# Optimization experiments

Measured on AMD Instinct MI355X. Metric: run time of the kernel, lower is better.

The kernel has to match this reference:

```python
import jax, jax.numpy as jnp
import numpy as np

B, S, D = 32, 512, 768
M, T = 32, 30
H, DFF, L, E = 12, 3072, 4, 100000
HD = D // H


def _layer_norm(x, w, b):
    m = jnp.mean(x, axis=-1, keepdims=True)
    v = jnp.var(x, axis=-1, keepdims=True)
    return (x - m) * jax.lax.rsqrt(v + 1e-5) * w + b


def _encoder_layer(x, p):
    # torch.nn.TransformerEncoderLayer, batch_first, post-LN, relu, eval (no dropout)
    wi, bi, wo, bo, g1, b1, w1, c1, w2, c2, g2, b2 = p
    qkv = x @ wi.T + bi                                   # [B,M,3D]
    q, k, v = jnp.split(qkv, 3, axis=-1)
    q = q.reshape(B, M, H, HD)
    k = k.reshape(B, M, H, HD)
    v = v.reshape(B, M, H, HD)
    a = jnp.einsum('bqhd,bkhd->bhqk', q, k) / np.float32(np.sqrt(HD))
    a = jax.nn.softmax(a, axis=-1)
    o = jnp.einsum('bhqk,bkhd->bqhd', a, v).reshape(B, M, D)
    x = _layer_norm(x + o @ wo.T + bo, g1, b1)
    ff = jax.nn.relu(x @ w1.T + c1) @ w2.T + c2
    return _layer_norm(x + ff, g2, b2)


def _forward(lhs, attn_w, attn_b, Wi, Bi, Wo, Bo, G1, B1, W1, C1, W2, C2, G2, B2v,
             cls_w1, cls_w2, cls_b2, pos, emask):
    # Vectorized form of the source triple loop: token slot x of mention (i,j) is
    # copied from last_hidden_state[i, x] while no -1 has been seen (break) and
    # the mention is active (entity_attention_mask != 0).
    valid = jnp.cumprod((pos != -1).astype(jnp.int32), axis=-1) > 0      # [B,M,T]
    valid = valid & (emask[:, :, None] != 0)
    mentions = jnp.where(valid[..., None], lhs[:, None, :T, :], 0.0)     # [B,M,T,D]
    scores = jax.nn.softmax(jnp.einsum('bmtd,d->bmt', mentions, attn_w) + attn_b, axis=-1)
    x = jnp.einsum('bmt,bmtd->bmd', scores, mentions)                    # attention pool
    for l in range(L):
        x = _encoder_layer(x, (Wi[l], Bi[l], Wo[l], Bo[l], G1[l], B1[l],
                               W1[l], C1[l], W2[l], C2[l], G2[l], B2v[l]))
    return (x @ cls_w1.T) @ cls_w2.T + cls_b2                            # [B,M,E]


def setup_inputs() -> dict:
    key = jax.random.key(0)
    k = jax.random.split(key, 12)
    lhs = jax.random.normal(k[0], (B, S, D), jnp.float32)
    pos = jax.random.randint(k[1], (B, M, T), 0, S)
    lens = jax.random.randint(k[2], (B, M), 0, T + 1)
    pos = jnp.where(jnp.arange(T)[None, None, :] < lens[..., None], pos, -1)
    emask = jax.random.randint(k[3], (B, M), 0, 2)
    s = 0.02
    return {
        'last_hidden_state': lhs,
        'attn_w': jax.random.normal(k[4], (D,), jnp.float32) * s,
        'attn_b': jnp.zeros((), jnp.float32),
        'in_proj_w': jax.random.normal(k[5], (L, 3 * D, D), jnp.float32) * s,
        'in_proj_b': jnp.zeros((L, 3 * D), jnp.float32),
        'out_w': jax.random.normal(k[6], (L, D, D), jnp.float32) * s,
        'out_b': jnp.zeros((L, D), jnp.float32),
        'ln1_w': jnp.ones((L, D), jnp.float32),
        'ln1_b': jnp.zeros((L, D), jnp.float32),
        'lin1_w': jax.random.normal(k[7], (L, DFF, D), jnp.float32) * s,
        'lin1_b': jnp.zeros((L, DFF), jnp.float32),
        'lin2_w': jax.random.normal(k[8], (L, D, DFF), jnp.float32) * s,
        'lin2_b': jnp.zeros((L, D), jnp.float32),
        'ln2_w': jnp.ones((L, D), jnp.float32),
        'ln2_b': jnp.zeros((L, D), jnp.float32),
        'cls_w1': jax.random.normal(k[9], (100, D), jnp.float32) * s,
        'cls_w2': jax.random.normal(k[10], (E, 100), jnp.float32) * s,
        'cls_b2': jnp.zeros((E,), jnp.float32),
        'entity_position_ids': pos,
        'entity_attention_mask': emask,
    }


def reference(last_hidden_state, attn_w, attn_b, in_proj_w, in_proj_b, out_w, out_b,
              ln1_w, ln1_b, lin1_w, lin1_b, lin2_w, lin2_b, ln2_w, ln2_b,
              cls_w1, cls_w2, cls_b2, entity_position_ids, entity_attention_mask):
    return _forward(last_hidden_state, attn_w, attn_b, in_proj_w, in_proj_b, out_w, out_b,
                    ln1_w, ln1_b, lin1_w, lin1_b, lin2_w, lin2_b, ln2_w, ln2_b,
                    cls_w1, cls_w2, cls_b2, entity_position_ids, entity_attention_mask)
```

## Files before the change

kernel.cpp:

```cpp
#include <hip/hip_runtime.h>

constexpr int Bc = 32, Sc = 512, Dc = 768, Mc = 32, Tc = 30;
constexpr int Hc = 12, DFFc = 3072, Lc = 4, Ec = 100000, HDc = 64;
constexpr int TOK = Bc * Mc;
constexpr int KC2 = 128;

typedef float floatx4 __attribute__((ext_vector_type(4)));
typedef __bf16 bfrag8 __attribute__((ext_vector_type(8)));
typedef unsigned short usx8 __attribute__((ext_vector_type(8)));
typedef unsigned short usx4 __attribute__((ext_vector_type(4)));

__device__ __forceinline__ unsigned short f32_to_bf16(float f) {
    unsigned int u = __float_as_uint(f);
    unsigned int r = (u + 0x7FFFu + ((u >> 16) & 1u)) >> 16;
    return (unsigned short)r;
}

__device__ __forceinline__ void gload_lds16(const void* gsrc, void* lds) {
    __builtin_amdgcn_global_load_lds((const unsigned int*)gsrc, (unsigned int*)lds, 16, 0, 0);
}

struct CvtSegs {
    const float* src[7];
    unsigned short* dst[7];
    unsigned int end[7];
    unsigned int total;
};

__global__ __launch_bounds__(256)
void cvt_multi_kernel(CvtSegs a) {
    const unsigned int stride = gridDim.x * 256;
    for (unsigned int i = blockIdx.x * 256 + threadIdx.x; i < a.total; i += stride) {
        int s = 0;
        while (i >= a.end[s]) ++s;
        const unsigned int off = i - (s ? a.end[s - 1] : 0u);
        usx4 o = (usx4)0;
        if (a.src[s]) {
            floatx4 v = *(const floatx4*)(a.src[s] + 4 * (size_t)off);
            #pragma unroll
            for (int j = 0; j < 4; ++j) o[j] = f32_to_bf16(v[j]);
        }
        *(usx4*)(a.dst[s] + 4 * (size_t)off) = o;
    }
}

__global__ __launch_bounds__(256)
void cvt_c2_kernel(const float* __restrict__ src, unsigned short* __restrict__ dst) {
    const int total = Ec * (KC2 / 8);
    const int stride = gridDim.x * 256;
    for (int c = blockIdx.x * 256 + threadIdx.x; c < total; c += stride) {
        const int row = c >> 4, j = c & 15;
        const int col0 = j * 8;
        const float* sp = src + (size_t)row * 100 + col0;
        usx8 o = (usx8)0;
        if (col0 + 8 <= 100) {
            floatx4 v0 = *(const floatx4*)(sp);
            floatx4 v1 = *(const floatx4*)(sp + 4);
            #pragma unroll
            for (int jj = 0; jj < 4; ++jj) { o[jj] = f32_to_bf16(v0[jj]); o[4 + jj] = f32_to_bf16(v1[jj]); }
        } else if (col0 < 100) {
            #pragma unroll
            for (int jj = 0; jj < 8; ++jj)
                if (col0 + jj < 100) o[jj] = f32_to_bf16(sp[jj]);
        }
        *(usx8*)(dst + (size_t)row * KC2 + col0) = o;
    }
}

__global__ __launch_bounds__(256)
void pool_kernel(const float* __restrict__ lhs, const float* __restrict__ attn_w,
                 const int* __restrict__ pos, const int* __restrict__ emask,
                 float* __restrict__ x0, unsigned short* __restrict__ x0b) {
    const int bm = blockIdx.x;
    const int b = bm >> 5;
    const int tid = threadIdx.x;
    __shared__ float s_logit[32];
    __shared__ float s_w[32];
    __shared__ int s_valid[32];

    if (tid == 0) {
        int em = emask[bm];
        int ok = 1;
        for (int t = 0; t < Tc; ++t) {
            if (pos[bm * Tc + t] == -1) ok = 0;
            s_valid[t] = (ok && em) ? 1 : 0;
        }
    }
    __syncthreads();

    const int wid = tid >> 6, lane = tid & 63;
    for (int t = wid; t < Tc; t += 4) {
        float p = 0.f;
        const float* row = lhs + ((size_t)b * Sc + t) * Dc;
        for (int d = lane; d < Dc; d += 64) p += row[d] * attn_w[d];
        #pragma unroll
        for (int off = 32; off > 0; off >>= 1) p += __shfl_down(p, off);
        if (lane == 0) s_logit[t] = s_valid[t] ? p : 0.0f;
    }
    __syncthreads();
    if (tid == 0) {
        float mx = -1e30f;
        for (int t = 0; t < Tc; ++t) mx = fmaxf(mx, s_logit[t]);
        float sum = 0.f;
        for (int t = 0; t < Tc; ++t) { float e = expf(s_logit[t] - mx); s_w[t] = e; sum += e; }
        float inv = 1.0f / sum;
        for (int t = 0; t < Tc; ++t) s_w[t] = s_valid[t] ? s_w[t] * inv : 0.0f;
    }
    __syncthreads();
    for (int d = tid; d < Dc; d += 256) {
        float acc = 0.f;
        for (int t = 0; t < Tc; ++t) acc += s_w[t] * lhs[((size_t)b * Sc + t) * Dc + d];
        x0[(size_t)bm * Dc + d] = acc;
        x0b[(size_t)bm * Dc + d] = f32_to_bf16(acc);
    }
}

template <int BM, int BN, int WM, int WN, int OUTBF>
__global__ __launch_bounds__(256)
void gemm_bf16_kernel(const unsigned short* __restrict__ A, int lda,
                      const unsigned short* __restrict__ B, int ldb,
                      const float* __restrict__ bias, void* __restrict__ Cv,
                      int ldc, int M, int N, int K, int relu, int nxReal) {
    constexpr int BK = 64;
    __shared__ unsigned short lA[BM * BK];
    __shared__ unsigned short lB[BN * BK];

    int bx, by;
    if (nxReal > 0) {
        const int gx = gridDim.x, gy = gridDim.y;
        const int lb = blockIdx.y * gx + blockIdx.x;
        const int xcd = lb & 7, p = lb >> 3;
        const int pq = p / gy;
        bx = xcd * (gx >> 3) + pq;
        by = p - pq * gy;
        if (bx >= nxReal) return;
    } else {
        bx = blockIdx.x; by = blockIdx.y;
    }
    const int z = blockIdx.z;
    A += (size_t)z * K;
    B += (size_t)z * K;

    const int tid = threadIdx.x;
    const int bm0 = by * BM;
    const int bn0 = bx * BN;

    const int wid = tid >> 6;
    const int lane = tid & 63;
    const int quad = lane >> 4;
    const int l16 = lane & 15;
    const int wr = (wid >> 1) * (WM * 16);
    const int wc = (wid & 1) * (WN * 16);

    floatx4 acc[WM][WN] = {};

    for (int k0 = 0; k0 < K; k0 += BK) {
        #pragma unroll
        for (int it = 0; it < BM / 32; ++it) {
            const int chunk = wid * (BM / 32) + it;
            const int boff = chunk * 1024 + lane * 16;
            const int row = boff >> 7;
            const int cb = (boff & 127) ^ ((row & 7) << 4);
            gload_lds16((const char*)(A + (size_t)(bm0 + row) * lda + k0) + cb,
                        &lA[chunk * 512]);
        }
        #pragma unroll
        for (int it = 0; it < BN / 32; ++it) {
            const int chunk = wid * (BN / 32) + it;
            const int boff = chunk * 1024 + lane * 16;
            const int row = boff >> 7;
            const int cb = (boff & 127) ^ ((row & 7) << 4);
            gload_lds16((const char*)(B + (size_t)(bn0 + row) * ldb + k0) + cb,
                        &lB[chunk * 512]);
        }
        __syncthreads();
        #pragma unroll
        for (int kk = 0; kk < BK; kk += 32) {
            bfrag8 af[WM], bfr[WN];
            #pragma unroll
            for (int i = 0; i < WM; ++i) {
                const int rowA = wr + i * 16 + l16;
                af[i] = *(const bfrag8*)((const char*)lA + rowA * 128 +
                                         ((kk * 2 + quad * 16) ^ ((rowA & 7) << 4)));
            }
            #pragma unroll
            for (int j = 0; j < WN; ++j) {
                const int rowB = wc + j * 16 + l16;
                bfr[j] = *(const bfrag8*)((const char*)lB + rowB * 128 +
                                          ((kk * 2 + quad * 16) ^ ((rowB & 7) << 4)));
            }
            #pragma unroll
            for (int i = 0; i < WM; ++i)
                #pragma unroll
                for (int j = 0; j < WN; ++j)
                    acc[i][j] = __builtin_amdgcn_mfma_f32_16x16x32_bf16(af[i], bfr[j], acc[i][j], 0, 0, 0);
        }
        __syncthreads();
    }

    #pragma unroll
    for (int i = 0; i < WM; ++i) {
        #pragma unroll
        for (int j = 0; j < WN; ++j) {
            const int col = bn0 + wc + j * 16 + l16;
            if (col < N) {
                const int row0 = bm0 + wr + i * 16 + quad * 4;
                const float bv = bias ? bias[col] : 0.0f;
                #pragma unroll
                for (int r = 0; r < 4; ++r) {
                    float v = acc[i][j][r] + bv;
                    if (relu) v = fmaxf(v, 0.0f);
                    const size_t idx = (size_t)z * M * ldc + (size_t)(row0 + r) * ldc + col;
                    if (OUTBF) ((unsigned short*)Cv)[idx] = f32_to_bf16(v);
                    else       ((float*)Cv)[idx] = v;
                }
            }
        }
    }
}

__global__ __launch_bounds__(256)
void attn_kernel(const float* __restrict__ qkv, unsigned short* __restrict__ outb) {
    const int bh = blockIdx.x;
    const int b = bh / Hc, h = bh % Hc;
    const int tid = threadIdx.x;
    __shared__ float sQ[32][65];
    __shared__ float sK[32][65];
    __shared__ float sV[32][65];
    __shared__ float sS[32][33];

    const int m = tid >> 3;
    const int c0 = (tid & 7) * 8;
    {
        const size_t rbase = ((size_t)(b * 32 + m)) * (3 * Dc);
        #pragma unroll
        for (int j = 0; j < 8; ++j) {
            sQ[m][c0 + j] = qkv[rbase + h * HDc + c0 + j];
            sK[m][c0 + j] = qkv[rbase + Dc + h * HDc + c0 + j];
            sV[m][c0 + j] = qkv[rbase + 2 * Dc + h * HDc + c0 + j];
        }
    }
    __syncthreads();

    #pragma unroll
    for (int u = 0; u < 4; ++u) {
        const int e = tid * 4 + u;
        const int q = e >> 5, k = e & 31;
        float s = 0.f;
        #pragma unroll
        for (int d = 0; d < HDc; ++d) s += sQ[q][d] * sK[k][d];
        sS[q][k] = s * 0.125f;
    }
    __syncthreads();
    if (tid < 32) {
        float mx = -1e30f;
        for (int k = 0; k < 32; ++k) mx = fmaxf(mx, sS[tid][k]);
        float sum = 0.f;
        for (int k = 0; k < 32; ++k) { float e = expf(sS[tid][k] - mx); sS[tid][k] = e; sum += e; }
        const float inv = 1.0f / sum;
        for (int k = 0; k < 32; ++k) sS[tid][k] *= inv;
    }
    __syncthreads();
    float o[8] = {};
    for (int k = 0; k < 32; ++k) {
        const float p = sS[m][k];
        #pragma unroll
        for (int j = 0; j < 8; ++j) o[j] += p * sV[k][c0 + j];
    }
    usx8 o8;
    #pragma unroll
    for (int j = 0; j < 8; ++j) o8[j] = f32_to_bf16(o[j]);
    *(usx8*)(&outb[((size_t)(b * 32 + m)) * Dc + h * HDc + c0]) = o8;
}

__global__ __launch_bounds__(256)
void addln_kernel(const float* __restrict__ xa, const float* __restrict__ xs, int nslab,
                  const float* __restrict__ badd, const float* __restrict__ g,
                  const float* __restrict__ be, float* __restrict__ outf,
                  unsigned short* __restrict__ outb) {
    const int row = blockIdx.x;
    const int tid = threadIdx.x;
    __shared__ float red[8];
    float v[3];
    float s = 0.f, sq = 0.f;
    #pragma unroll
    for (int i = 0; i < 3; ++i) {
        const int d = tid + i * 256;
        float x = xa[(size_t)row * Dc + d] + badd[d];
        for (int sl = 0; sl < nslab; ++sl)
            x += xs[((size_t)sl * TOK + row) * Dc + d];
        v[i] = x; s += x; sq += x * x;
    }
    #pragma unroll
    for (int off = 32; off > 0; off >>= 1) {
        s += __shfl_down(s, off);
        sq += __shfl_down(sq, off);
    }
    if ((tid & 63) == 0) { red[tid >> 6] = s; red[4 + (tid >> 6)] = sq; }
    __syncthreads();
    const float ts = red[0] + red[1] + red[2] + red[3];
    const float tq = red[4] + red[5] + red[6] + red[7];
    const float mean = ts * (1.0f / Dc);
    const float var = tq * (1.0f / Dc) - mean * mean;
    const float inv = rsqrtf(var + 1e-5f);
    #pragma unroll
    for (int i = 0; i < 3; ++i) {
        const int d = tid + i * 256;
        const float y = (v[i] - mean) * inv * g[d] + be[d];
        outf[(size_t)row * Dc + d] = y;
        outb[(size_t)row * Dc + d] = f32_to_bf16(y);
    }
}

extern "C" void kernel_launch(void* const* d_in, const int* in_sizes, int n_in,
                              void* d_out, int out_size, void* d_ws, size_t ws_size,
                              hipStream_t stream) {
    const float* lhs   = (const float*)d_in[0];
    const float* attnw = (const float*)d_in[1];
    const float* ipw = (const float*)d_in[3];
    const float* ipb = (const float*)d_in[4];
    const float* oww = (const float*)d_in[5];
    const float* owb = (const float*)d_in[6];
    const float* g1  = (const float*)d_in[7];
    const float* b1  = (const float*)d_in[8];
    const float* l1w = (const float*)d_in[9];
    const float* l1b = (const float*)d_in[10];
    const float* l2w = (const float*)d_in[11];
    const float* l2b = (const float*)d_in[12];
    const float* g2  = (const float*)d_in[13];
    const float* b2  = (const float*)d_in[14];
    const float* cw1 = (const float*)d_in[15];
    const float* cw2 = (const float*)d_in[16];
    const float* cb2 = (const float*)d_in[17];
    const int* pos   = (const int*)d_in[18];
    const int* emask = (const int*)d_in[19];
    float* out = (float*)d_out;

    constexpr size_t N_IP = (size_t)Lc * 3 * Dc * Dc;
    constexpr size_t N_OW = (size_t)Lc * Dc * Dc;
    constexpr size_t N_L1 = (size_t)Lc * DFFc * Dc;
    constexpr size_t N_L2 = (size_t)Lc * Dc * DFFc;
    constexpr size_t N_C1 = (size_t)KC2 * Dc;

    char* ws = (char*)d_ws;
    unsigned short* bw_c2 = (unsigned short*)ws;
    unsigned short* bufCb = bw_c2 + (size_t)Ec * KC2;

    constexpr size_t F_XA   = (size_t)TOK * Dc;
    constexpr size_t F_QKV  = (size_t)TOK * 3 * Dc;
    constexpr size_t F_SLAB = (size_t)4 * TOK * Dc;
    constexpr size_t S_ACT  = (size_t)TOK * Dc;
    constexpr size_t S_FFH  = (size_t)TOK * DFFc;
    constexpr size_t tail_bytes =
        4 * (F_XA + F_XA + F_QKV + F_SLAB) +
        2 * (N_IP + N_OW + N_L1 + N_L2 + N_C1 + 3 * S_ACT + S_FFH);

    const size_t out_bytes = (size_t)out_size * 4;
    char* tail = (char*)d_out + ((out_bytes - tail_bytes) & ~(size_t)255);

    float* xA   = (float*)tail;
    float* xB   = xA + F_XA;
    float* qkvb = xB + F_XA;
    float* bufS = qkvb + F_QKV;
    unsigned short* bw_ip = (unsigned short*)(bufS + F_SLAB);
    unsigned short* bw_ow = bw_ip + N_IP;
    unsigned short* bw_l1 = bw_ow + N_OW;
    unsigned short* bw_l2 = bw_l1 + N_L1;
    unsigned short* bw_c1 = bw_l2 + N_L2;
    unsigned short* xAb   = bw_c1 + N_C1;
    unsigned short* xBb   = xAb + S_ACT;
    unsigned short* attnb = xBb + S_ACT;
    unsigned short* bufHb = attnb + S_ACT;

    {
        CvtSegs segs{};
        const float* srcs[6] = {ipw, oww, l1w, l2w, cw1, nullptr};
        unsigned short* dsts[6] = {bw_ip, bw_ow, bw_l1, bw_l2, bw_c1, bw_c1 + (size_t)100 * Dc};
        const unsigned int cnt[6] = {(unsigned)(N_IP / 4), (unsigned)(N_OW / 4),
                                     (unsigned)(N_L1 / 4), (unsigned)(N_L2 / 4),
                                     (unsigned)(100 * Dc / 4), (unsigned)(28 * Dc / 4)};
        unsigned int acc = 0;
        for (int i = 0; i < 6; ++i) { segs.src[i] = srcs[i]; segs.dst[i] = dsts[i]; acc += cnt[i]; segs.end[i] = acc; }
        segs.src[6] = nullptr; segs.dst[6] = dsts[5]; segs.end[6] = 0xFFFFFFFFu;
        segs.total = acc;
        cvt_multi_kernel<<<2048, 256, 0, stream>>>(segs);
    }
    cvt_c2_kernel<<<1024, 256, 0, stream>>>(cw2, bw_c2);

    pool_kernel<<<TOK, 256, 0, stream>>>(lhs, attnw, pos, emask, xA, xAb);

    auto g64 = [&](const unsigned short* A, int lda, const unsigned short* B, int ldb,
                   const float* bias, void* C, int ldc, int N, int K, int relu,
                   int ks, int outbf, bool swz) {
        int gx = (N + 63) / 64, nx = -1;
        if (swz) { nx = gx; gx = (gx + 7) & ~7; }
        dim3 grid(gx, TOK / 64, ks);
        if (outbf) gemm_bf16_kernel<64, 64, 2, 2, 1><<<grid, 256, 0, stream>>>(A, lda, B, ldb, bias, C, ldc, TOK, N, K, relu, nx);
        else       gemm_bf16_kernel<64, 64, 2, 2, 0><<<grid, 256, 0, stream>>>(A, lda, B, ldb, bias, C, ldc, TOK, N, K, relu, nx);
    };

    for (int l = 0; l < Lc; ++l) {
        g64(xAb, Dc, bw_ip + (size_t)l * 3 * Dc * Dc, Dc, ipb + (size_t)l * 3 * Dc,
            qkvb, 3 * Dc, 3 * Dc, Dc, 0, 1, 0, false);
        attn_kernel<<<Bc * Hc, 256, 0, stream>>>(qkvb, attnb);
        g64(attnb, Dc, bw_ow + (size_t)l * Dc * Dc, Dc, nullptr,
            bufS, Dc, Dc, Dc / 4, 0, 4, 0, false);
        addln_kernel<<<TOK, 256, 0, stream>>>(xA, bufS, 4, owb + (size_t)l * Dc,
                                              g1 + (size_t)l * Dc, b1 + (size_t)l * Dc, xB, xBb);
        g64(xBb, Dc, bw_l1 + (size_t)l * DFFc * Dc, Dc, l1b + (size_t)l * DFFc,
            bufHb, DFFc, DFFc, Dc, 1, 1, 1, true);
        g64(bufHb, DFFc, bw_l2 + (size_t)l * Dc * DFFc, DFFc, nullptr,
            bufS, Dc, Dc, DFFc / 4, 0, 4, 0, false);
        addln_kernel<<<TOK, 256, 0, stream>>>(xB, bufS, 4, l2b + (size_t)l * Dc,
                                              g2 + (size_t)l * Dc, b2 + (size_t)l * Dc, xA, xAb);
    }

    g64(xAb, Dc, bw_c1, Dc, nullptr, bufCb, KC2, KC2, Dc, 0, 1, 1, false);
    {
        int nx = (Ec + 127) / 128;
        int gx = (nx + 7) & ~7;
        dim3 grid(gx, TOK / 128, 1);
        gemm_bf16_kernel<128, 128, 4, 4, 0><<<grid, 256, 0, stream>>>(
            bufCb, KC2, bw_c2, KC2, cb2, out, Ec, TOK, Ec, KC2, 0, nx);
    }
}
```

Baseline: 1.000 ms.

## Merge front conversion/pool kernels and double-buffer GEMM LDS tiles

Combines the two weight-conversion kernels and the mention pooling kernel into one launch, with blocks split by index range, which removes two launches and lets the independent work run side by side. The GEMM kernel also gets double-buffered LDS: the next K tile is loaded with global_load_lds while MFMA runs on the current tile, and one barrier per iteration is dropped. This doubles LDS use per block, which may lower occupancy. There is no explicit wait on the asynchronous LDS loads before the barrier, so correctness relies on the compiler inserting the right waitcnt.

```diff
diff --git a/kernel.cpp b/kernel.cpp
--- a/kernel.cpp
+++ b/kernel.cpp
@@ -27,53 +27,57 @@
     unsigned int total;
 };
 
+constexpr int FB_CVT1 = 1536, FB_CVT2 = 512, FB_POOL = TOK;
+
 __global__ __launch_bounds__(256)
-void cvt_multi_kernel(CvtSegs a) {
-    const unsigned int stride = gridDim.x * 256;
-    for (unsigned int i = blockIdx.x * 256 + threadIdx.x; i < a.total; i += stride) {
-        int s = 0;
-        while (i >= a.end[s]) ++s;
-        const unsigned int off = i - (s ? a.end[s - 1] : 0u);
-        usx4 o = (usx4)0;
-        if (a.src[s]) {
-            floatx4 v = *(const floatx4*)(a.src[s] + 4 * (size_t)off);
-            #pragma unroll
-            for (int j = 0; j < 4; ++j) o[j] = f32_to_bf16(v[j]);
-        }
-        *(usx4*)(a.dst[s] + 4 * (size_t)off) = o;
-    }
-}
-
-__global__ __launch_bounds__(256)
-void cvt_c2_kernel(const float* __restrict__ src, unsigned short* __restrict__ dst) {
-    const int total = Ec * (KC2 / 8);
-    const int stride = gridDim.x * 256;
-    for (int c = blockIdx.x * 256 + threadIdx.x; c < total; c += stride) {
-        const int row = c >> 4, j = c & 15;
-        const int col0 = j * 8;
-        const float* sp = src + (size_t)row * 100 + col0;
-        usx8 o = (usx8)0;
-        if (col0 + 8 <= 100) {
-            floatx4 v0 = *(const floatx4*)(sp);
-            floatx4 v1 = *(const floatx4*)(sp + 4);
-            #pragma unroll
-            for (int jj = 0; jj < 4; ++jj) { o[jj] = f32_to_bf16(v0[jj]); o[4 + jj] = f32_to_bf16(v1[jj]); }
-        } else if (col0 < 100) {
-            #pragma unroll
-            for (int jj = 0; jj < 8; ++jj)
-                if (col0 + jj < 100) o[jj] = f32_to_bf16(sp[jj]);
-        }
-        *(usx8*)(dst + (size_t)row * KC2 + col0) = o;
-    }
-}
-
-__global__ __launch_bounds__(256)
-void pool_kernel(const float* __restrict__ lhs, const float* __restrict__ attn_w,
-                 const int* __restrict__ pos, const int* __restrict__ emask,
-                 float* __restrict__ x0, unsigned short* __restrict__ x0b) {
-    const int bm = blockIdx.x;
+void front_kernel(CvtSegs a, const float* __restrict__ cw2, unsigned short* __restrict__ bw_c2,
+                  const float* __restrict__ lhs, const float* __restrict__ attn_w,
+                  const int* __restrict__ pos, const int* __restrict__ emask,
+                  float* __restrict__ x0, unsigned short* __restrict__ x0b) {
+    const int bid = blockIdx.x;
+    const int tid = threadIdx.x;
+
+    if (bid < FB_CVT1) {
+        const unsigned int stride = FB_CVT1 * 256;
+        for (unsigned int i = bid * 256 + tid; i < a.total; i += stride) {
+            int s = 0;
+            while (i >= a.end[s]) ++s;
+            const unsigned int off = i - (s ? a.end[s - 1] : 0u);
+            usx4 o = (usx4)0;
+            if (a.src[s]) {
+                floatx4 v = *(const floatx4*)(a.src[s] + 4 * (size_t)off);
+                #pragma unroll
+                for (int j = 0; j < 4; ++j) o[j] = f32_to_bf16(v[j]);
+            }
+            *(usx4*)(a.dst[s] + 4 * (size_t)off) = o;
+        }
+        return;
+    }
+    if (bid < FB_CVT1 + FB_CVT2) {
+        const int total = Ec * (KC2 / 8);
+        const int stride = FB_CVT2 * 256;
+        for (int c = (bid - FB_CVT1) * 256 + tid; c < total; c += stride) {
+            const int row = c >> 4, j = c & 15;
+            const int col0 = j * 8;
+            const float* sp = cw2 + (size_t)row * 100 + col0;
+            usx8 o = (usx8)0;
+            if (col0 + 8 <= 100) {
+                floatx4 v0 = *(const floatx4*)(sp);
+                floatx4 v1 = *(const floatx4*)(sp + 4);
+                #pragma unroll
+                for (int jj = 0; jj < 4; ++jj) { o[jj] = f32_to_bf16(v0[jj]); o[4 + jj] = f32_to_bf16(v1[jj]); }
+            } else if (col0 < 100) {
+                #pragma unroll
+                for (int jj = 0; jj < 8; ++jj)
+                    if (col0 + jj < 100) o[jj] = f32_to_bf16(sp[jj]);
+            }
+            *(usx8*)(bw_c2 + (size_t)row * KC2 + col0) = o;
+        }
+        return;
+    }
+
+    const int bm = bid - (FB_CVT1 + FB_CVT2);
     const int b = bm >> 5;
-    const int tid = threadIdx.x;
     __shared__ float s_logit[32];
     __shared__ float s_w[32];
     __shared__ int s_valid[32];
@@ -122,8 +126,8 @@
                       const float* __restrict__ bias, void* __restrict__ Cv,
                       int ldc, int M, int N, int K, int relu, int nxReal) {
     constexpr int BK = 64;
-    __shared__ unsigned short lA[BM * BK];
-    __shared__ unsigned short lB[BN * BK];
+    __shared__ unsigned short lA[2][BM * BK];
+    __shared__ unsigned short lB[2][BN * BK];
 
     int bx, by;
     if (nxReal > 0) {
@@ -154,7 +158,7 @@
 
     floatx4 acc[WM][WN] = {};
 
-    for (int k0 = 0; k0 < K; k0 += BK) {
+    auto stageA = [&](int buf, int k0) {
         #pragma unroll
         for (int it = 0; it < BM / 32; ++it) {
             const int chunk = wid * (BM / 32) + it;
@@ -162,8 +166,10 @@
             const int row = boff >> 7;
             const int cb = (boff & 127) ^ ((row & 7) << 4);
             gload_lds16((const char*)(A + (size_t)(bm0 + row) * lda + k0) + cb,
-                        &lA[chunk * 512]);
-        }
+                        &lA[buf][chunk * 512]);
+        }
+    };
+    auto stageB = [&](int buf, int k0) {
         #pragma unroll
         for (int it = 0; it < BN / 32; ++it) {
             const int chunk = wid * (BN / 32) + it;
@@ -171,22 +177,34 @@
             const int row = boff >> 7;
             const int cb = (boff & 127) ^ ((row & 7) << 4);
             gload_lds16((const char*)(B + (size_t)(bn0 + row) * ldb + k0) + cb,
-                        &lB[chunk * 512]);
-        }
-        __syncthreads();
+                        &lB[buf][chunk * 512]);
+        }
+    };
+
+    stageA(0, 0);
+    stageB(0, 0);
+    __syncthreads();
+
+    int c = 0;
+    for (int k0 = 0; k0 < K; k0 += BK, c ^= 1) {
+        const int kn = k0 + BK;
+        const bool more = (kn < K);
+        if (more) { stageA(c ^ 1, kn); stageB(c ^ 1, kn); }
+        const unsigned short* bA = lA[c];
+        const unsigned short* bB = lB[c];
         #pragma unroll
         for (int kk = 0; kk < BK; kk += 32) {
             bfrag8 af[WM], bfr[WN];
             #pragma unroll
             for (int i = 0; i < WM; ++i) {
                 const int rowA = wr + i * 16 + l16;
-                af[i] = *(const bfrag8*)((const char*)lA + rowA * 128 +
+                af[i] = *(const bfrag8*)((const char*)bA + rowA * 128 +
                                          ((kk * 2 + quad * 16) ^ ((rowA & 7) << 4)));
             }
             #pragma unroll
             for (int j = 0; j < WN; ++j) {
                 const int rowB = wc + j * 16 + l16;
-                bfr[j] = *(const bfrag8*)((const char*)lB + rowB * 128 +
+                bfr[j] = *(const bfrag8*)((const char*)bB + rowB * 128 +
                                           ((kk * 2 + quad * 16) ^ ((rowB & 7) << 4)));
             }
             #pragma unroll
@@ -195,7 +213,7 @@
                 for (int j = 0; j < WN; ++j)
                     acc[i][j] = __builtin_amdgcn_mfma_f32_16x16x32_bf16(af[i], bfr[j], acc[i][j], 0, 0, 0);
         }
-        __syncthreads();
+        if (more) __syncthreads();
     }
 
     #pragma unroll
@@ -383,11 +401,9 @@
         for (int i = 0; i < 6; ++i) { segs.src[i] = srcs[i]; segs.dst[i] = dsts[i]; acc += cnt[i]; segs.end[i] = acc; }
         segs.src[6] = nullptr; segs.dst[6] = dsts[5]; segs.end[6] = 0xFFFFFFFFu;
         segs.total = acc;
-        cvt_multi_kernel<<<2048, 256, 0, stream>>>(segs);
-    }
-    cvt_c2_kernel<<<1024, 256, 0, stream>>>(cw2, bw_c2);
-
-    pool_kernel<<<TOK, 256, 0, stream>>>(lhs, attnw, pos, emask, xA, xAb);
+        front_kernel<<<FB_CVT1 + FB_CVT2 + FB_POOL, 256, 0, stream>>>(
+            segs, cw2, bw_c2, lhs, attnw, pos, emask, xA, xAb);
+    }
 
     auto g64 = [&](const unsigned short* A, int lda, const unsigned short* B, int ldb,
                    const float* bias, void* C, int ldc, int N, int K, int relu,
```

Measured after the change: 1.023 ms. +2.2%, slower.
